# Optimization experiments

Measured on AMD Instinct MI355X. Metric: run time of the kernel, lower is better.

## Reference

```python
import jax, jax.numpy as jnp
import numpy as np

N_NODES = 50000
N_EDGES = 800000
NODE_DIM = 64
EDGE_DIM = 32
HIDDEN_DIM = 128
OUT_DIM = 64


def setup_inputs() -> dict:
    key = jax.random.key(0)
    k1, k2, k3, k4, k5, k6, k7 = jax.random.split(key, 7)
    in_dim = EDGE_DIM + 2 * NODE_DIM  # 160
    edge_index = jax.random.randint(k1, (2, N_EDGES), 0, N_NODES, dtype=jnp.int64)
    node_features = jax.random.normal(k2, (N_NODES, NODE_DIM), dtype=jnp.float32)
    edge_features = jax.random.normal(k3, (N_EDGES, EDGE_DIM), dtype=jnp.float32)
    # MLP params (kaiming-uniform-ish init scale, values only matter for correctness testing)
    w1 = jax.random.normal(k4, (in_dim, HIDDEN_DIM), dtype=jnp.float32) * (1.0 / np.sqrt(in_dim))
    b1 = jax.random.normal(k5, (HIDDEN_DIM,), dtype=jnp.float32) * 0.01
    w2 = jax.random.normal(k6, (HIDDEN_DIM, OUT_DIM), dtype=jnp.float32) * (1.0 / np.sqrt(HIDDEN_DIM))
    b2 = jax.random.normal(k7, (OUT_DIM,), dtype=jnp.float32) * 0.01
    return {
        "edge_index": edge_index,
        "node_features": node_features,
        "edge_features": edge_features,
        "w1": w1, "b1": b1, "w2": w2, "b2": b2,
    }


def reference(edge_index, node_features, edge_features, w1, b1, w2, b2):
    # Gather source / target node features along the edge list: [E, NODE_DIM]
    src = node_features[edge_index[0]]
    tgt = node_features[edge_index[1]]
    # Concat to [E, EDGE_DIM + 2*NODE_DIM]
    x = jnp.concatenate([edge_features, src, tgt], axis=1)
    # 2-layer MLP: Linear -> ReLU -> Linear
    h = jax.nn.relu(x @ w1 + b1)
    return h @ w2 + b2
```

## Files before the change

kernel.cpp:

```cpp
#include <hip/hip_runtime.h>

#define E_TOTAL 800000
#define NN      50000
#define ND      64
#define ED      32
#define HD      128
#define OD      64
#define IND     160
#define MT      128
#define NTHREADS 512
#define NT      (E_TOTAL / MT)
#define GRID    512

typedef __attribute__((ext_vector_type(8))) short          short8;
typedef __attribute__((ext_vector_type(4))) float          f32x4;
typedef __attribute__((ext_vector_type(8))) unsigned short u16x8;
typedef __attribute__((ext_vector_type(4))) unsigned short u16x4;

__device__ __forceinline__ unsigned short f2bf(float f) {
  union { float f; unsigned u; } v; v.f = f;
  unsigned r = v.u + 0x7fffu + ((v.u >> 16) & 1u);
  return (unsigned short)(r >> 16);
}

#define H_FRAGS  32
#define SMEM_U16 ((H_FRAGS + 40) * 512)
#define SMEM_BYTES (SMEM_U16 * 2)

__global__ void cvt_nodes(const float* __restrict__ in, unsigned short* __restrict__ out, int n4) {
  int i = blockIdx.x * blockDim.x + threadIdx.x;
  const int stride = gridDim.x * blockDim.x;
  for (; i < n4; i += stride) {
    float4 v = ((const float4*)in)[i];
    u16x4 o = { f2bf(v.x), f2bf(v.y), f2bf(v.z), f2bf(v.w) };
    ((u16x4*)out)[i] = o;
  }
}

__global__ void pack_w1(const float* __restrict__ w, unsigned short* __restrict__ out) {
  int i = blockIdx.x * blockDim.x + threadIdx.x;
  if (i >= HD * IND) return;
  int j = i & 7, l = (i >> 3) & 63, f = i >> 9;
  int ks = f >> 3, t = f & 7;
  int k = ks * 32 + (l >> 4) * 8 + j;
  int n = t * 16 + (l & 15);
  out[i] = f2bf(w[k * HD + n]);
}

__global__ void pack_w2(const float* __restrict__ w, unsigned short* __restrict__ out) {
  int i = blockIdx.x * blockDim.x + threadIdx.x;
  if (i >= OD * HD) return;
  int j = i & 7, l = (i >> 3) & 63, f = i >> 9;
  int ks = f >> 2, t = f & 3;
  int k = ks * 32 + (l >> 4) * 8 + j;
  int n = t * 16 + (l & 15);
  out[i] = f2bf(w[k * OD + n]);
}

__global__ __launch_bounds__(NTHREADS, 4)
void edge_mlp(const int* __restrict__ eidx,
              const float* __restrict__ ef,
              const unsigned short* __restrict__ nbf,
              const unsigned short* __restrict__ w1p,
              const unsigned short* __restrict__ w2p,
              const float* __restrict__ b1,
              const float* __restrict__ b2,
              float* __restrict__ out)
{
  extern __shared__ unsigned short sm[];
  unsigned short* Hs = sm;
  unsigned short* W1 = sm + H_FRAGS * 512;

  const int tid  = threadIdx.x;
  const int wid  = tid >> 6;
  const int lane = tid & 63;
  const int lq   = lane >> 4;
  const int lr   = lane & 15;
  const int rowoff = wid * 16 + lr;

  #pragma unroll
  for (int c = 0; c < 5; ++c) {
    const int i = tid + c * NTHREADS;
    *(u16x8*)(W1 + i * 8) = *(const u16x8*)(w1p + i * 8);
  }

  float b1v[8];
  #pragma unroll
  for (int t = 0; t < 8; ++t) b1v[t] = b1[t * 16 + lr];
  float b2v[4];
  #pragma unroll
  for (int t = 0; t < 4; ++t) b2v[t] = b2[t * 16 + lr];

  int tile = blockIdx.x;
  short8 g0, g1, g2, g3;
  float4 e0v, e1v;
  {
    const long e = (long)tile * MT + rowoff;
    int si = eidx[e];           si = si < 0 ? 0 : (si >= NN ? NN - 1 : si);
    int ti = eidx[E_TOTAL + e]; ti = ti < 0 ? 0 : (ti >= NN ? NN - 1 : ti);
    const unsigned short* sr = nbf + (long)si * ND;
    const unsigned short* tr = nbf + (long)ti * ND;
    g0 = *(const short8*)(sr + lq * 8);
    g1 = *(const short8*)(sr + 32 + lq * 8);
    g2 = *(const short8*)(tr + lq * 8);
    g3 = *(const short8*)(tr + 32 + lq * 8);
    e0v = *(const float4*)(ef + e * ED + lq * 8);
    e1v = *(const float4*)(ef + e * ED + lq * 8 + 4);
  }

  asm volatile("s_waitcnt lgkmcnt(0)" ::: "memory");
  __builtin_amdgcn_s_barrier();
  __builtin_amdgcn_sched_barrier(0);

  for (; tile < NT; tile += GRID) {
    const int  tnext = (tile + GRID < NT) ? (tile + GRID) : tile;
    const long en    = (long)tnext * MT + rowoff;
    int sn = eidx[en];
    int tn = eidx[E_TOTAL + en];

    short8 aef;
    aef[0] = (short)f2bf(e0v.x); aef[1] = (short)f2bf(e0v.y);
    aef[2] = (short)f2bf(e0v.z); aef[3] = (short)f2bf(e0v.w);
    aef[4] = (short)f2bf(e1v.x); aef[5] = (short)f2bf(e1v.y);
    aef[6] = (short)f2bf(e1v.z); aef[7] = (short)f2bf(e1v.w);

    f32x4 acc[8];
    #pragma unroll
    for (int t = 0; t < 8; ++t) acc[t] = (f32x4)0.0f;

    #pragma unroll
    for (int ks = 0; ks < 5; ++ks) {
      const short8 a = (ks == 0) ? aef : (ks == 1) ? g0 : (ks == 2) ? g1
                        : (ks == 3) ? g2 : g3;
      #pragma unroll
      for (int t = 0; t < 8; ++t) {
        const short8 b = *(const short8*)(W1 + (ks * 8 + t) * 512 + lane * 8);
        acc[t] = __builtin_amdgcn_mfma_f32_16x16x32_bf16(a, b, acc[t], 0, 0, 0);
      }
    }

    asm volatile("s_waitcnt lgkmcnt(0)" ::: "memory");
    __builtin_amdgcn_s_barrier();
    __builtin_amdgcn_sched_barrier(0);

    #pragma unroll
    for (int t = 0; t < 8; ++t) {
      #pragma unroll
      for (int r = 0; r < 4; ++r) {
        float h = acc[t][r] + b1v[t];
        h = h > 0.0f ? h : 0.0f;
        const int k    = t * 16 + lr;
        const int frag = wid * 4 + (k >> 5);
        const int l2   = (((k >> 3) & 3) << 4) + lq * 4 + r;
        Hs[frag * 512 + l2 * 8 + (k & 7)] = f2bf(h);
      }
    }

    asm volatile("s_waitcnt lgkmcnt(0)" ::: "memory");
    __builtin_amdgcn_s_barrier();
    __builtin_amdgcn_sched_barrier(0);

    short8 a2[4];
    #pragma unroll
    for (int ks = 0; ks < 4; ++ks)
      a2[ks] = *(const short8*)(Hs + (wid * 4 + ks) * 512 + lane * 8);

    sn = sn < 0 ? 0 : (sn >= NN ? NN - 1 : sn);
    tn = tn < 0 ? 0 : (tn >= NN ? NN - 1 : tn);
    {
      const unsigned short* sr = nbf + (long)sn * ND;
      const unsigned short* tr = nbf + (long)tn * ND;
      g0 = *(const short8*)(sr + lq * 8);
      g1 = *(const short8*)(sr + 32 + lq * 8);
      g2 = *(const short8*)(tr + lq * 8);
      g3 = *(const short8*)(tr + 32 + lq * 8);
      e0v = *(const float4*)(ef + en * ED + lq * 8);
      e1v = *(const float4*)(ef + en * ED + lq * 8 + 4);
    }

    f32x4 acc2[4];
    #pragma unroll
    for (int t = 0; t < 4; ++t) acc2[t] = (f32x4)0.0f;
    #pragma unroll
    for (int t = 0; t < 4; ++t) {
      #pragma unroll
      for (int ks = 0; ks < 4; ++ks) {
        const short8 b = *(const short8*)(w2p + ((ks * 4 + t) * 64 + lane) * 8);
        acc2[t] = __builtin_amdgcn_mfma_f32_16x16x32_bf16(a2[ks], b, acc2[t], 0, 0, 0);
      }
    }

    const long mbase = (long)tile * MT + wid * 16 + lq * 4;
    #pragma unroll
    for (int t = 0; t < 4; ++t) {
      #pragma unroll
      for (int r = 0; r < 4; ++r) {
        out[(mbase + r) * OD + t * 16 + lr] = acc2[t][r] + b2v[t];
      }
    }
  }
}

extern "C" void kernel_launch(void* const* d_in, const int* in_sizes, int n_in,
                              void* d_out, int out_size, void* d_ws, size_t ws_size,
                              hipStream_t stream) {
  const int*   eidx = (const int*)d_in[0];
  const float* nf   = (const float*)d_in[1];
  const float* ef   = (const float*)d_in[2];
  const float* w1   = (const float*)d_in[3];
  const float* b1   = (const float*)d_in[4];
  const float* w2   = (const float*)d_in[5];
  const float* b2   = (const float*)d_in[6];
  float*       out  = (float*)d_out;

  unsigned short* nbf = (unsigned short*)d_ws;
  unsigned short* w1p = nbf + (long)NN * ND;
  unsigned short* w2p = w1p + (long)HD * IND;

  cvt_nodes<<<1024, 256, 0, stream>>>(nf, nbf, (NN * ND) / 4);
  pack_w1<<<(HD * IND + 255) / 256, 256, 0, stream>>>(w1, w1p);
  pack_w2<<<(OD * HD + 255) / 256, 256, 0, stream>>>(w2, w2p);

  hipFuncSetAttribute((const void*)edge_mlp,
                      hipFuncAttributeMaxDynamicSharedMemorySize, SMEM_BYTES);
  edge_mlp<<<GRID, NTHREADS, SMEM_BYTES, stream>>>(
      eidx, ef, nbf, w1p, w2p, b1, b2, out);
}
```

Baseline: 140.4 us.

## Drop per-tile block barriers and prefetch edge indices two tiles ahead

Removes the two workgroup barriers inside the tile loop. Each wave writes and reads only its own fragments of the hidden-activation LDS buffer, so cross-wave synchronisation is not needed there. Moves the next tile's node-feature and edge-feature gathers to just after the layer-1 MFMAs, loads edge indices two tiles ahead so the gather addresses are ready earlier, and runs the edge-feature MFMA step last. The aim is to remove barrier stalls and hide gather latency, at the cost of more live registers and reliance on same-wave LDS ordering for correctness.

Result: slower. 166.6 us (+18.7%).

```diff
diff --git a/kernel.cpp b/kernel.cpp
--- a/kernel.cpp
+++ b/kernel.cpp
@@ -91,7 +91,10 @@
   #pragma unroll
   for (int t = 0; t < 4; ++t) b2v[t] = b2[t * 16 + lr];
 
+  __syncthreads();
+
   int tile = blockIdx.x;
+
   short8 g0, g1, g2, g3;
   float4 e0v, e1v;
   {
@@ -107,17 +110,16 @@
     e0v = *(const float4*)(ef + e * ED + lq * 8);
     e1v = *(const float4*)(ef + e * ED + lq * 8 + 4);
   }
-
-  asm volatile("s_waitcnt lgkmcnt(0)" ::: "memory");
-  __builtin_amdgcn_s_barrier();
-  __builtin_amdgcn_sched_barrier(0);
+  long eNxt;
+  int  sN, tN;
+  {
+    const int tnext = (tile + GRID < NT) ? (tile + GRID) : tile;
+    eNxt = (long)tnext * MT + rowoff;
+    sN = eidx[eNxt];
+    tN = eidx[E_TOTAL + eNxt];
+  }
 
   for (; tile < NT; tile += GRID) {
-    const int  tnext = (tile + GRID < NT) ? (tile + GRID) : tile;
-    const long en    = (long)tnext * MT + rowoff;
-    int sn = eidx[en];
-    int tn = eidx[E_TOTAL + en];
-
     short8 aef;
     aef[0] = (short)f2bf(e0v.x); aef[1] = (short)f2bf(e0v.y);
     aef[2] = (short)f2bf(e0v.z); aef[3] = (short)f2bf(e0v.w);
@@ -128,20 +130,37 @@
     #pragma unroll
     for (int t = 0; t < 8; ++t) acc[t] = (f32x4)0.0f;
 
-    #pragma unroll
-    for (int ks = 0; ks < 5; ++ks) {
-      const short8 a = (ks == 0) ? aef : (ks == 1) ? g0 : (ks == 2) ? g1
-                        : (ks == 3) ? g2 : g3;
-      #pragma unroll
-      for (int t = 0; t < 8; ++t) {
-        const short8 b = *(const short8*)(W1 + (ks * 8 + t) * 512 + lane * 8);
-        acc[t] = __builtin_amdgcn_mfma_f32_16x16x32_bf16(a, b, acc[t], 0, 0, 0);
-      }
-    }
-
-    asm volatile("s_waitcnt lgkmcnt(0)" ::: "memory");
-    __builtin_amdgcn_s_barrier();
-    __builtin_amdgcn_sched_barrier(0);
+    #define L1STEP(AV, KS)                                                     \
+      _Pragma("unroll")                                                        \
+      for (int t = 0; t < 8; ++t) {                                            \
+        const short8 b = *(const short8*)(W1 + ((KS) * 8 + t) * 512 + lane * 8); \
+        acc[t] = __builtin_amdgcn_mfma_f32_16x16x32_bf16(AV, b, acc[t], 0, 0, 0); \
+      }
+    L1STEP(g0, 1)
+    L1STEP(g1, 2)
+    L1STEP(g2, 3)
+    L1STEP(g3, 4)
+    L1STEP(aef, 0)
+    #undef L1STEP
+
+    {
+      int si = sN < 0 ? 0 : (sN >= NN ? NN - 1 : sN);
+      int ti = tN < 0 ? 0 : (tN >= NN ? NN - 1 : tN);
+      const unsigned short* sr = nbf + (long)si * ND;
+      const unsigned short* tr = nbf + (long)ti * ND;
+      g0 = *(const short8*)(sr + lq * 8);
+      g1 = *(const short8*)(sr + 32 + lq * 8);
+      g2 = *(const short8*)(tr + lq * 8);
+      g3 = *(const short8*)(tr + 32 + lq * 8);
+      e0v = *(const float4*)(ef + eNxt * ED + lq * 8);
+      e1v = *(const float4*)(ef + eNxt * ED + lq * 8 + 4);
+    }
+    {
+      const int tn2 = (tile + 2 * GRID < NT) ? (tile + 2 * GRID) : tile;
+      eNxt = (long)tn2 * MT + rowoff;
+      sN = eidx[eNxt];
+      tN = eidx[E_TOTAL + eNxt];
+    }
 
     #pragma unroll
     for (int t = 0; t < 8; ++t) {
@@ -156,27 +175,10 @@
       }
     }
 
-    asm volatile("s_waitcnt lgkmcnt(0)" ::: "memory");
-    __builtin_amdgcn_s_barrier();
-    __builtin_amdgcn_sched_barrier(0);
-
     short8 a2[4];
     #pragma unroll
     for (int ks = 0; ks < 4; ++ks)
       a2[ks] = *(const short8*)(Hs + (wid * 4 + ks) * 512 + lane * 8);
-
-    sn = sn < 0 ? 0 : (sn >= NN ? NN - 1 : sn);
-    tn = tn < 0 ? 0 : (tn >= NN ? NN - 1 : tn);
-    {
-      const unsigned short* sr = nbf + (long)sn * ND;
-      const unsigned short* tr = nbf + (long)tn * ND;
-      g0 = *(const short8*)(sr + lq * 8);
-      g1 = *(const short8*)(sr + 32 + lq * 8);
-      g2 = *(const short8*)(tr + lq * 8);
-      g3 = *(const short8*)(tr + 32 + lq * 8);
-      e0v = *(const float4*)(ef + en * ED + lq * 8);
-      e1v = *(const float4*)(ef + en * ED + lq * 8 + 4);
-    }
 
     f32x4 acc2[4];
     #pragma unroll
```

## Double-buffer edge gathers in registers and drop intra-tile barriers

Applied to the files above, without the earlier changes.

The tile loop becomes a two-way register ping-pong. The node-feature and edge-feature gathers for the next tile are issued before the current tile's MFMA work, and the index loads are prefetched two tiles ahead. The block-wide barriers around the hidden-activation LDS round trip are removed, since each wave writes and reads only its own fragments. This aims to hide gather latency and cut synchronisation, but the second set of gather registers raises VGPR pressure under the 4-block launch bound and could cause spills.

Result: slower. 192.7 us (+37.3%).

```diff
diff --git a/kernel.cpp b/kernel.cpp
--- a/kernel.cpp
+++ b/kernel.cpp
@@ -91,114 +91,127 @@
   #pragma unroll
   for (int t = 0; t < 4; ++t) b2v[t] = b2[t * 16 + lr];
 
+  __syncthreads();
+
+  #define GATHER(G0,G1,G2,G3,EV0,EV1, SI, TI, EOFF)                         \
+    {                                                                        \
+      int si_ = (SI); si_ = si_ < 0 ? 0 : (si_ >= NN ? NN - 1 : si_);        \
+      int ti_ = (TI); ti_ = ti_ < 0 ? 0 : (ti_ >= NN ? NN - 1 : ti_);        \
+      const unsigned short* sr_ = nbf + (long)si_ * ND;                      \
+      const unsigned short* tr_ = nbf + (long)ti_ * ND;                      \
+      G0 = *(const short8*)(sr_ + lq * 8);                                   \
+      G1 = *(const short8*)(sr_ + 32 + lq * 8);                              \
+      G2 = *(const short8*)(tr_ + lq * 8);                                   \
+      G3 = *(const short8*)(tr_ + 32 + lq * 8);                              \
+      EV0 = *(const float4*)(ef + (long)(EOFF) * ED + lq * 8);               \
+      EV1 = *(const float4*)(ef + (long)(EOFF) * ED + lq * 8 + 4);           \
+    }
+
+  #define COMPUTE(G0,G1,G2,G3,EV0,EV1, TILE)                                 \
+    {                                                                        \
+      short8 aef;                                                            \
+      aef[0] = (short)f2bf(EV0.x); aef[1] = (short)f2bf(EV0.y);              \
+      aef[2] = (short)f2bf(EV0.z); aef[3] = (short)f2bf(EV0.w);              \
+      aef[4] = (short)f2bf(EV1.x); aef[5] = (short)f2bf(EV1.y);              \
+      aef[6] = (short)f2bf(EV1.z); aef[7] = (short)f2bf(EV1.w);              \
+      f32x4 acc[8];                                                          \
+      _Pragma("unroll")                                                      \
+      for (int t = 0; t < 8; ++t) acc[t] = (f32x4)0.0f;                      \
+      _Pragma("unroll")                                                      \
+      for (int t = 0; t < 8; ++t) {                                          \
+        const short8 b = *(const short8*)(W1 + (1 * 8 + t) * 512 + lane * 8);\
+        acc[t] = __builtin_amdgcn_mfma_f32_16x16x32_bf16(G0, b, acc[t], 0, 0, 0); } \
+      _Pragma("unroll")                                                      \
+      for (int t = 0; t < 8; ++t) {                                          \
+        const short8 b = *(const short8*)(W1 + (2 * 8 + t) * 512 + lane * 8);\
+        acc[t] = __builtin_amdgcn_mfma_f32_16x16x32_bf16(G1, b, acc[t], 0, 0, 0); } \
+      _Pragma("unroll")                                                      \
+      for (int t = 0; t < 8; ++t) {                                          \
+        const short8 b = *(const short8*)(W1 + (3 * 8 + t) * 512 + lane * 8);\
+        acc[t] = __builtin_amdgcn_mfma_f32_16x16x32_bf16(G2, b, acc[t], 0, 0, 0); } \
+      _Pragma("unroll")                                                      \
+      for (int t = 0; t < 8; ++t) {                                          \
+        const short8 b = *(const short8*)(W1 + (4 * 8 + t) * 512 + lane * 8);\
+        acc[t] = __builtin_amdgcn_mfma_f32_16x16x32_bf16(G3, b, acc[t], 0, 0, 0); } \
+      _Pragma("unroll")                                                      \
+      for (int t = 0; t < 8; ++t) {                                          \
+        const short8 b = *(const short8*)(W1 + (0 * 8 + t) * 512 + lane * 8);\
+        acc[t] = __builtin_amdgcn_mfma_f32_16x16x32_bf16(aef, b, acc[t], 0, 0, 0); } \
+      _Pragma("unroll")                                                      \
+      for (int t = 0; t < 8; ++t) {                                          \
+        _Pragma("unroll")                                                    \
+        for (int r = 0; r < 4; ++r) {                                        \
+          float h = acc[t][r] + b1v[t];                                      \
+          h = h > 0.0f ? h : 0.0f;                                           \
+          const int k    = t * 16 + lr;                                      \
+          const int frag = wid * 4 + (k >> 5);                               \
+          const int l2   = (((k >> 3) & 3) << 4) + lq * 4 + r;               \
+          Hs[frag * 512 + l2 * 8 + (k & 7)] = f2bf(h);                       \
+        }                                                                    \
+      }                                                                      \
+      short8 a2[4];                                                          \
+      _Pragma("unroll")                                                      \
+      for (int ks = 0; ks < 4; ++ks)                                         \
+        a2[ks] = *(const short8*)(Hs + (wid * 4 + ks) * 512 + lane * 8);     \
+      f32x4 acc2[4];                                                         \
+      _Pragma("unroll")                                                      \
+      for (int t = 0; t < 4; ++t) acc2[t] = (f32x4)0.0f;                     \
+      _Pragma("unroll")                                                      \
+      for (int t = 0; t < 4; ++t) {                                          \
+        _Pragma("unroll")                                                    \
+        for (int ks = 0; ks < 4; ++ks) {                                     \
+          const short8 b = *(const short8*)(w2p + ((ks * 4 + t) * 64 + lane) * 8); \
+          acc2[t] = __builtin_amdgcn_mfma_f32_16x16x32_bf16(a2[ks], b, acc2[t], 0, 0, 0); } } \
+      const long mbase = (long)(TILE) * MT + wid * 16 + lq * 4;              \
+      _Pragma("unroll")                                                      \
+      for (int t = 0; t < 4; ++t) {                                          \
+        _Pragma("unroll")                                                    \
+        for (int r = 0; r < 4; ++r) {                                        \
+          out[(mbase + r) * OD + t * 16 + lr] = acc2[t][r] + b2v[t];         \
+        }                                                                    \
+      }                                                                      \
+    }
+
   int tile = blockIdx.x;
-  short8 g0, g1, g2, g3;
-  float4 e0v, e1v;
+
+  short8 gA0, gA1, gA2, gA3;  float4 eA0, eA1;
+  short8 gB0, gB1, gB2, gB3;  float4 eB0, eB1;
   {
-    const long e = (long)tile * MT + rowoff;
-    int si = eidx[e];           si = si < 0 ? 0 : (si >= NN ? NN - 1 : si);
-    int ti = eidx[E_TOTAL + e]; ti = ti < 0 ? 0 : (ti >= NN ? NN - 1 : ti);
-    const unsigned short* sr = nbf + (long)si * ND;
-    const unsigned short* tr = nbf + (long)ti * ND;
-    g0 = *(const short8*)(sr + lq * 8);
-    g1 = *(const short8*)(sr + 32 + lq * 8);
-    g2 = *(const short8*)(tr + lq * 8);
-    g3 = *(const short8*)(tr + 32 + lq * 8);
-    e0v = *(const float4*)(ef + e * ED + lq * 8);
-    e1v = *(const float4*)(ef + e * ED + lq * 8 + 4);
-  }
-
-  asm volatile("s_waitcnt lgkmcnt(0)" ::: "memory");
-  __builtin_amdgcn_s_barrier();
-  __builtin_amdgcn_sched_barrier(0);
-
-  for (; tile < NT; tile += GRID) {
-    const int  tnext = (tile + GRID < NT) ? (tile + GRID) : tile;
-    const long en    = (long)tnext * MT + rowoff;
-    int sn = eidx[en];
-    int tn = eidx[E_TOTAL + en];
-
-    short8 aef;
-    aef[0] = (short)f2bf(e0v.x); aef[1] = (short)f2bf(e0v.y);
-    aef[2] = (short)f2bf(e0v.z); aef[3] = (short)f2bf(e0v.w);
-    aef[4] = (short)f2bf(e1v.x); aef[5] = (short)f2bf(e1v.y);
-    aef[6] = (short)f2bf(e1v.z); aef[7] = (short)f2bf(e1v.w);
-
-    f32x4 acc[8];
-    #pragma unroll
-    for (int t = 0; t < 8; ++t) acc[t] = (f32x4)0.0f;
-
-    #pragma unroll
-    for (int ks = 0; ks < 5; ++ks) {
-      const short8 a = (ks == 0) ? aef : (ks == 1) ? g0 : (ks == 2) ? g1
-                        : (ks == 3) ? g2 : g3;
-      #pragma unroll
-      for (int t = 0; t < 8; ++t) {
-        const short8 b = *(const short8*)(W1 + (ks * 8 + t) * 512 + lane * 8);
-        acc[t] = __builtin_amdgcn_mfma_f32_16x16x32_bf16(a, b, acc[t], 0, 0, 0);
-      }
-    }
-
-    asm volatile("s_waitcnt lgkmcnt(0)" ::: "memory");
+    const int e = tile * MT + rowoff;
+    GATHER(gA0, gA1, gA2, gA3, eA0, eA1, eidx[e], eidx[E_TOTAL + e], e);
+  }
+  int eoff1, sN1, tN1, eoff2, sN2, tN2;
+  {
+    int tn = tile + GRID; if (tn >= NT) tn = NT - 1;
+    eoff1 = tn * MT + rowoff;
+    sN1 = eidx[eoff1]; tN1 = eidx[E_TOTAL + eoff1];
+  }
+
+  for (; tile + GRID < NT; tile += 2 * GRID) {
     __builtin_amdgcn_s_barrier();
-    __builtin_amdgcn_sched_barrier(0);
-
-    #pragma unroll
-    for (int t = 0; t < 8; ++t) {
-      #pragma unroll
-      for (int r = 0; r < 4; ++r) {
-        float h = acc[t][r] + b1v[t];
-        h = h > 0.0f ? h : 0.0f;
-        const int k    = t * 16 + lr;
-        const int frag = wid * 4 + (k >> 5);
-        const int l2   = (((k >> 3) & 3) << 4) + lq * 4 + r;
-        Hs[frag * 512 + l2 * 8 + (k & 7)] = f2bf(h);
-      }
-    }
-
-    asm volatile("s_waitcnt lgkmcnt(0)" ::: "memory");
+    GATHER(gB0, gB1, gB2, gB3, eB0, eB1, sN1, tN1, eoff1);
+    {
+      int tn = tile + 2 * GRID; if (tn >= NT) tn = NT - 1;
+      eoff2 = tn * MT + rowoff;
+      sN2 = eidx[eoff2]; tN2 = eidx[E_TOTAL + eoff2];
+    }
+    COMPUTE(gA0, gA1, gA2, gA3, eA0, eA1, tile);
+
     __builtin_amdgcn_s_barrier();
-    __builtin_amdgcn_sched_barrier(0);
-
-    short8 a2[4];
-    #pragma unroll
-    for (int ks = 0; ks < 4; ++ks)
-      a2[ks] = *(const short8*)(Hs + (wid * 4 + ks) * 512 + lane * 8);
-
-    sn = sn < 0 ? 0 : (sn >= NN ? NN - 1 : sn);
-    tn = tn < 0 ? 0 : (tn >= NN ? NN - 1 : tn);
+    GATHER(gA0, gA1, gA2, gA3, eA0, eA1, sN2, tN2, eoff2);
     {
-      const unsigned short* sr = nbf + (long)sn * ND;
-      const unsigned short* tr = nbf + (long)tn * ND;
-      g0 = *(const short8*)(sr + lq * 8);
-      g1 = *(const short8*)(sr + 32 + lq * 8);
-      g2 = *(const short8*)(tr + lq * 8);
-      g3 = *(const short8*)(tr + 32 + lq * 8);
-      e0v = *(const float4*)(ef + en * ED + lq * 8);
-      e1v = *(const float4*)(ef + en * ED + lq * 8 + 4);
-    }
-
-    f32x4 acc2[4];
-    #pragma unroll
-    for (int t = 0; t < 4; ++t) acc2[t] = (f32x4)0.0f;
-    #pragma unroll
-    for (int t = 0; t < 4; ++t) {
-      #pragma unroll
-      for (int ks = 0; ks < 4; ++ks) {
-        const short8 b = *(const short8*)(w2p + ((ks * 4 + t) * 64 + lane) * 8);
-        acc2[t] = __builtin_amdgcn_mfma_f32_16x16x32_bf16(a2[ks], b, acc2[t], 0, 0, 0);
-      }
-    }
-
-    const long mbase = (long)tile * MT + wid * 16 + lq * 4;
-    #pragma unroll
-    for (int t = 0; t < 4; ++t) {
-      #pragma unroll
-      for (int r = 0; r < 4; ++r) {
-        out[(mbase + r) * OD + t * 16 + lr] = acc2[t][r] + b2v[t];
-      }
-    }
-  }
+      int tn = tile + 3 * GRID; if (tn >= NT) tn = NT - 1;
+      eoff1 = tn * MT + rowoff;
+      sN1 = eidx[eoff1]; tN1 = eidx[E_TOTAL + eoff1];
+    }
+    COMPUTE(gB0, gB1, gB2, gB3, eB0, eB1, tile + GRID);
+  }
+  if (tile < NT) {
+    COMPUTE(gA0, gA1, gA2, gA3, eA0, eA1, tile);
+  }
+
+  #undef GATHER
+  #undef COMPUTE
 }
 
 extern "C" void kernel_launch(void* const* d_in, const int* in_sizes, int n_in,
```
